# Kernel tuning notes

Hardware: AMD Instinct MI355X
Metric: run time of the kernel (lower is better)

## Reference

```python
import jax, jax.numpy as jnp
import numpy as np

HEADS = 16
HEAD_DIM = 64
LN_EPS = 1e-5


def setup_inputs() -> dict:
    key = jax.random.key(0)
    k_x, k_q, k_k, k_v = jax.random.split(key, 4)
    B, C, H, W = 32, 640, 32, 32
    inner = HEADS * HEAD_DIM  # 1024
    x = jax.random.normal(k_x, (B, C, H, W), dtype=jnp.float32)
    # nn.Linear(in_dim, inner_dim, bias=False): weight shape [inner, in_dim]
    Wq = jax.random.normal(k_q, (inner, C), dtype=jnp.float32) * 0.02
    Wk = jax.random.normal(k_k, (inner, C), dtype=jnp.float32) * 0.02
    Wv = jax.random.normal(k_v, (inner, C), dtype=jnp.float32) * 0.02
    # out_norm = nn.LayerNorm(head_dim): default init gamma=1, beta=0
    gamma = jnp.ones((HEAD_DIM,), dtype=jnp.float32)
    beta = jnp.zeros((HEAD_DIM,), dtype=jnp.float32)
    return {"x": x, "Wq": Wq, "Wk": Wk, "Wv": Wv, "gamma": gamma, "beta": beta}


def _layernorm(y, gamma, beta):
    mu = jnp.mean(y, axis=-1, keepdims=True)
    var = jnp.mean(jnp.square(y - mu), axis=-1, keepdims=True)
    return (y - mu) * jax.lax.rsqrt(var + LN_EPS) * gamma + beta


def reference(x, Wq, Wk, Wv, gamma, beta):
    B, C, H, W = x.shape
    N = H * W
    scale = HEAD_DIM ** -0.5
    # rearrange 'b c h w -> b (h w) c' (patch_size=1)
    t = x.reshape(B, C, N).transpose(0, 2, 1)  # [B, N, C]
    def proj(Wm):
        p = jnp.einsum('bnc,ec->bne', t, Wm)  # [B, N, inner]
        return p.reshape(B, N, HEADS, HEAD_DIM).transpose(0, 2, 1, 3)  # [B, h, N, d]
    q, k, v = proj(Wq), proj(Wk), proj(Wv)
    qk = jnp.einsum('bhid,bhjd->bhij', q, k)  # [B, h, N, N]
    p_att = jax.nn.softmax(qk * scale, axis=-1)
    out = jnp.einsum('bhij,bhjd->bhid', p_att, v)  # [B, h, N, d]
    out = out.mean(axis=2)  # [B, h, d]
    return _layernorm(out, gamma, beta)
```

## Files before the change

### kernel.cpp

```cpp
#include <hip/hip_runtime.h>
#include <hip/hip_bf16.h>

typedef __bf16 bf16;
typedef __bf16 bf16x8 __attribute__((ext_vector_type(8)));
typedef float f32x4 __attribute__((ext_vector_type(4)));

#define QSCALE 0.18033688011112042f

#define EXP2(x) __builtin_amdgcn_exp2f(x)

__device__ __forceinline__ void load_lds16(const void* gp, void* lp) {
  __builtin_amdgcn_global_load_lds((const __attribute__((address_space(1))) void*)gp,
                                   (__attribute__((address_space(3))) void*)lp, 16, 0, 0);
}

__global__ __launch_bounds__(256) void k_transpose(const float* __restrict__ x,
                                                   bf16* __restrict__ t) {
  __shared__ float tile[64][65];
  const int b = blockIdx.z, c0 = blockIdx.y * 64, n0 = blockIdx.x * 64;
  const int tid = threadIdx.x, lx = tid & 63, ly = tid >> 6;
  const float* xp = x + ((size_t)b * 640 + c0) * 1024 + n0;
#pragma unroll
  for (int i = 0; i < 16; ++i) {
    int c = i * 4 + ly;
    tile[c][lx] = xp[(size_t)c * 1024 + lx];
  }
  __syncthreads();
  bf16* tp = t + ((size_t)b * 1024 + n0) * 640 + c0;
#pragma unroll
  for (int i = 0; i < 16; ++i) {
    int n = i * 4 + ly;
    tp[(size_t)n * 640 + lx] = (bf16)tile[lx][n];
  }
}

__global__ __launch_bounds__(256) void k_castw(const float* __restrict__ w,
                                               bf16* __restrict__ dst, float s) {
  int i = blockIdx.x * 256 + threadIdx.x;
  if (i < 655360) dst[i] = (bf16)(w[i] * s);
}

__global__ __launch_bounds__(256) void k_gemm_qkv(const bf16* __restrict__ A,
                                                  const bf16* __restrict__ Bw,
                                                  bf16* __restrict__ qkv) {
  __shared__ __align__(16) bf16 As[128 * 64];
  __shared__ __align__(16) bf16 Bs[128 * 64];
  const int tid = threadIdx.x;
  const int lane = tid & 63;
  const int w = tid >> 6;
  const int wm = w & 1, wn = w >> 1;
  const int g = lane >> 4, ln = lane & 15;
  const int m0 = blockIdx.x * 128;
  const int n0 = blockIdx.y * 128;

  f32x4 acc[4][4];
#pragma unroll
  for (int i = 0; i < 4; ++i)
#pragma unroll
    for (int j = 0; j < 4; ++j)
#pragma unroll
      for (int r = 0; r < 4; ++r) acc[i][j][r] = 0.f;

  for (int k0 = 0; k0 < 640; k0 += 64) {
#pragma unroll
    for (int it = 0; it < 4; ++it) {
      int c = it * 256 + w * 64 + lane;
      int m = c >> 3;
      int kq = (c & 7) ^ (m & 7);
      load_lds16(A + (size_t)(m0 + m) * 640 + (k0 + kq * 8), As + (size_t)(it * 256 + w * 64) * 8);
      load_lds16(Bw + (size_t)(n0 + m) * 640 + (k0 + kq * 8), Bs + (size_t)(it * 256 + w * 64) * 8);
    }
    __syncthreads();
#pragma unroll
    for (int kk = 0; kk < 2; ++kk) {
      bf16x8 af[4], bfr[4];
#pragma unroll
      for (int mi = 0; mi < 4; ++mi) {
        int m = wm * 64 + mi * 16 + ln;
        int cc = m * 8 + ((kk * 4 + g) ^ (m & 7));
        af[mi] = *(const bf16x8*)(As + cc * 8);
      }
#pragma unroll
      for (int ni = 0; ni < 4; ++ni) {
        int n = wn * 64 + ni * 16 + ln;
        int cc = n * 8 + ((kk * 4 + g) ^ (n & 7));
        bfr[ni] = *(const bf16x8*)(Bs + cc * 8);
      }
#pragma unroll
      for (int mi = 0; mi < 4; ++mi)
#pragma unroll
        for (int ni = 0; ni < 4; ++ni)
          acc[mi][ni] = __builtin_amdgcn_mfma_f32_16x16x32_bf16(af[mi], bfr[ni], acc[mi][ni], 0, 0, 0);
    }
    __syncthreads();
  }

#pragma unroll
  for (int mi = 0; mi < 4; ++mi)
#pragma unroll
    for (int ni = 0; ni < 4; ++ni)
#pragma unroll
      for (int r = 0; r < 4; ++r) {
        int row = m0 + wm * 64 + mi * 16 + g * 4 + r;
        int col = n0 + wn * 64 + ni * 16 + ln;
        int bb = row >> 10, n = row & 1023;
        int which = col >> 10, h = (col >> 6) & 15, d = col & 63;
        qkv[(size_t)which * 33554432 +
            ((((size_t)bb * 16 + h) * 1024 + n) * 64 + d)] = (bf16)acc[mi][ni][r];
      }
}

__global__ __launch_bounds__(256) void k_attn(const bf16* __restrict__ q,
                                              const bf16* __restrict__ kmat,
                                              float* __restrict__ wsum) {
  const int bh = blockIdx.y;
  const int it = blockIdx.x;
  const int tid = threadIdx.x;
  const int lane = tid & 63;
  const int w = tid >> 6;
  const int g = lane >> 4, ln = lane & 15;
  const bf16* qb = q + (size_t)bh * 65536;
  const bf16* kb = kmat + (size_t)bh * 65536;
  const int i0 = it * 256 + w * 64;

  bf16x8 qf[4][2];
#pragma unroll
  for (int mi = 0; mi < 4; ++mi)
#pragma unroll
    for (int kc = 0; kc < 2; ++kc)
      qf[mi][kc] = *(const bf16x8*)(qb + (size_t)(i0 + mi * 16 + ln) * 64 + kc * 32 + g * 8);

  float rs[4][4];
#pragma unroll
  for (int mi = 0; mi < 4; ++mi)
#pragma unroll
    for (int r = 0; r < 4; ++r) rs[mi][r] = 0.f;

  for (int jt = 0; jt < 16; ++jt) {
    bf16x8 kf[4][2];
#pragma unroll
    for (int ni = 0; ni < 4; ++ni)
#pragma unroll
      for (int kc = 0; kc < 2; ++kc)
        kf[ni][kc] = *(const bf16x8*)(kb + (size_t)(jt * 64 + ni * 16 + ln) * 64 + kc * 32 + g * 8);
#pragma unroll
    for (int mi = 0; mi < 4; ++mi)
#pragma unroll
      for (int ni = 0; ni < 4; ++ni) {
        f32x4 s = {0.f, 0.f, 0.f, 0.f};
        s = __builtin_amdgcn_mfma_f32_16x16x32_bf16(qf[mi][0], kf[ni][0], s, 0, 0, 0);
        s = __builtin_amdgcn_mfma_f32_16x16x32_bf16(qf[mi][1], kf[ni][1], s, 0, 0, 0);
#pragma unroll
        for (int r = 0; r < 4; ++r) rs[mi][r] += EXP2(s[r]);
      }
  }
  float rinv[4][4];
#pragma unroll
  for (int mi = 0; mi < 4; ++mi)
#pragma unroll
    for (int r = 0; r < 4; ++r) {
      float v = rs[mi][r];
      v += __shfl_xor(v, 1);
      v += __shfl_xor(v, 2);
      v += __shfl_xor(v, 4);
      v += __shfl_xor(v, 8);
      rinv[mi][r] = 1.0f / v;
    }

  for (int jt = 0; jt < 16; ++jt) {
    bf16x8 kf[4][2];
#pragma unroll
    for (int ni = 0; ni < 4; ++ni)
#pragma unroll
      for (int kc = 0; kc < 2; ++kc)
        kf[ni][kc] = *(const bf16x8*)(kb + (size_t)(jt * 64 + ni * 16 + ln) * 64 + kc * 32 + g * 8);
    float cs[4] = {0.f, 0.f, 0.f, 0.f};
#pragma unroll
    for (int mi = 0; mi < 4; ++mi)
#pragma unroll
      for (int ni = 0; ni < 4; ++ni) {
        f32x4 s = {0.f, 0.f, 0.f, 0.f};
        s = __builtin_amdgcn_mfma_f32_16x16x32_bf16(qf[mi][0], kf[ni][0], s, 0, 0, 0);
        s = __builtin_amdgcn_mfma_f32_16x16x32_bf16(qf[mi][1], kf[ni][1], s, 0, 0, 0);
#pragma unroll
        for (int r = 0; r < 4; ++r) cs[ni] += EXP2(s[r]) * rinv[mi][r];
      }
#pragma unroll
    for (int ni = 0; ni < 4; ++ni) {
      float v = cs[ni];
      v += __shfl_xor(v, 16);
      v += __shfl_xor(v, 32);
      if (g == 0) atomicAdd(wsum + (size_t)bh * 1024 + jt * 64 + ni * 16 + ln, v);
    }
  }
}

__global__ __launch_bounds__(256) void k_final(const float* __restrict__ wsum,
                                               const bf16* __restrict__ v,
                                               const float* __restrict__ gamma,
                                               const float* __restrict__ beta,
                                               float* __restrict__ out) {
  const int bh = blockIdx.x;
  const int tid = threadIdx.x;
  const int d = tid & 63, part = tid >> 6;
  const bf16* vb = v + (size_t)bh * 65536;
  const float* wb = wsum + (size_t)bh * 1024;
  float acc = 0.f;
  for (int j = part * 256; j < part * 256 + 256; ++j)
    acc += wb[j] * (float)vb[(size_t)j * 64 + d];
  __shared__ float red[4][64];
  red[part][d] = acc;
  __syncthreads();
  if (tid < 64) {
    float y = (red[0][d] + red[1][d] + red[2][d] + red[3][d]) * (1.0f / 1024.0f);
    float s1 = y;
#pragma unroll
    for (int off = 1; off < 64; off <<= 1) s1 += __shfl_xor(s1, off);
    float mu = s1 * (1.0f / 64.0f);
    float dy = y - mu;
    float s2 = dy * dy;
#pragma unroll
    for (int off = 1; off < 64; off <<= 1) s2 += __shfl_xor(s2, off);
    float rstd = rsqrtf(s2 * (1.0f / 64.0f) + 1e-5f);
    out[(size_t)bh * 64 + d] = dy * rstd * gamma[d] + beta[d];
  }
}

extern "C" void kernel_launch(void* const* d_in, const int* in_sizes, int n_in,
                              void* d_out, int out_size, void* d_ws, size_t ws_size,
                              hipStream_t stream) {
  const float* x     = (const float*)d_in[0];
  const float* Wq    = (const float*)d_in[1];
  const float* Wk    = (const float*)d_in[2];
  const float* Wv    = (const float*)d_in[3];
  const float* gamma = (const float*)d_in[4];
  const float* beta  = (const float*)d_in[5];
  float* out = (float*)d_out;

  char* ws = (char*)d_ws;
  bf16*  tbf  = (bf16*)ws;
  bf16*  wbf  = (bf16*)(ws + 41943040);
  bf16*  qkv  = (bf16*)(ws + 45875200);
  float* wsum = (float*)(ws + 247201792);

  hipMemsetAsync(wsum, 0, (size_t)512 * 1024 * sizeof(float), stream);
  k_transpose<<<dim3(16, 10, 32), 256, 0, stream>>>(x, tbf);
  k_castw<<<2560, 256, 0, stream>>>(Wq, wbf, QSCALE);
  k_castw<<<2560, 256, 0, stream>>>(Wk, wbf + 655360, 1.0f);
  k_castw<<<2560, 256, 0, stream>>>(Wv, wbf + 1310720, 1.0f);
  k_gemm_qkv<<<dim3(256, 24), 256, 0, stream>>>(tbf, wbf, qkv);
  k_attn<<<dim3(4, 512), 256, 0, stream>>>(qkv, qkv + 33554432, wsum);
  k_final<<<512, 256, 0, stream>>>(wsum, qkv + 67108864, gamma, beta, out);
}
```

Baseline: 569.2 us.

## Double-buffer K fragment loads and remap attention blocks for XCD L2 locality

The attention kernel now prefetches the next K tile into a second register buffer while computing on the current one, in both the row-sum pass and the column-weight pass. The grid is flattened and remapped so that the four i-tiles of one batch-head land on the same XCD, which should let them share K reads in that XCD's L2. The double buffer raises register pressure and may lower occupancy.

```diff
diff --git a/kernel.cpp b/kernel.cpp
--- a/kernel.cpp
+++ b/kernel.cpp
@@ -110,11 +110,23 @@
       }
 }
 
+#define LOADK(buf, jt)                                                        \
+  do {                                                                        \
+    const bf16* kp_ = kb + (size_t)(jt) * 4096 + ln * 64 + g * 8;             \
+    _Pragma("unroll") for (int ni_ = 0; ni_ < 4; ++ni_) {                     \
+      buf[ni_ * 2 + 0] = *(const bf16x8*)(kp_ + ni_ * 1024);                  \
+      buf[ni_ * 2 + 1] = *(const bf16x8*)(kp_ + ni_ * 1024 + 32);             \
+    }                                                                         \
+  } while (0)
+
 __global__ __launch_bounds__(256) void k_attn(const bf16* __restrict__ q,
                                               const bf16* __restrict__ kmat,
                                               float* __restrict__ wsum) {
-  const int bh = blockIdx.y;
-  const int it = blockIdx.x;
+  const int idx = blockIdx.x;
+  const int xcd = idx & 7;
+  const int y = idx >> 3;
+  const int it = y & 3;
+  const int bh = xcd + ((y >> 2) << 3);
   const int tid = threadIdx.x;
   const int lane = tid & 63;
   const int w = tid >> 6;
@@ -123,6 +135,8 @@
   const bf16* kb = kmat + (size_t)bh * 65536;
   const int i0 = it * 256 + w * 64;
 
+  const f32x4 zf = {0.f, 0.f, 0.f, 0.f};
+
   bf16x8 qf[4][2];
 #pragma unroll
   for (int mi = 0; mi < 4; ++mi)
@@ -136,20 +150,18 @@
 #pragma unroll
     for (int r = 0; r < 4; ++r) rs[mi][r] = 0.f;
 
+  bf16x8 kbuf[2][8];
+
+  LOADK(kbuf[0], 0);
   for (int jt = 0; jt < 16; ++jt) {
-    bf16x8 kf[4][2];
-#pragma unroll
-    for (int ni = 0; ni < 4; ++ni)
-#pragma unroll
-      for (int kc = 0; kc < 2; ++kc)
-        kf[ni][kc] = *(const bf16x8*)(kb + (size_t)(jt * 64 + ni * 16 + ln) * 64 + kc * 32 + g * 8);
+    if (jt < 15) LOADK(kbuf[(jt + 1) & 1], jt + 1);
+    const bf16x8* kf = kbuf[jt & 1];
 #pragma unroll
     for (int mi = 0; mi < 4; ++mi)
 #pragma unroll
       for (int ni = 0; ni < 4; ++ni) {
-        f32x4 s = {0.f, 0.f, 0.f, 0.f};
-        s = __builtin_amdgcn_mfma_f32_16x16x32_bf16(qf[mi][0], kf[ni][0], s, 0, 0, 0);
-        s = __builtin_amdgcn_mfma_f32_16x16x32_bf16(qf[mi][1], kf[ni][1], s, 0, 0, 0);
+        f32x4 s = __builtin_amdgcn_mfma_f32_16x16x32_bf16(qf[mi][0], kf[ni * 2], zf, 0, 0, 0);
+        s = __builtin_amdgcn_mfma_f32_16x16x32_bf16(qf[mi][1], kf[ni * 2 + 1], s, 0, 0, 0);
 #pragma unroll
         for (int r = 0; r < 4; ++r) rs[mi][r] += EXP2(s[r]);
       }
@@ -167,21 +179,17 @@
       rinv[mi][r] = 1.0f / v;
     }
 
+  LOADK(kbuf[0], 0);
   for (int jt = 0; jt < 16; ++jt) {
-    bf16x8 kf[4][2];
-#pragma unroll
-    for (int ni = 0; ni < 4; ++ni)
-#pragma unroll
-      for (int kc = 0; kc < 2; ++kc)
-        kf[ni][kc] = *(const bf16x8*)(kb + (size_t)(jt * 64 + ni * 16 + ln) * 64 + kc * 32 + g * 8);
+    if (jt < 15) LOADK(kbuf[(jt + 1) & 1], jt + 1);
+    const bf16x8* kf = kbuf[jt & 1];
     float cs[4] = {0.f, 0.f, 0.f, 0.f};
 #pragma unroll
     for (int mi = 0; mi < 4; ++mi)
 #pragma unroll
       for (int ni = 0; ni < 4; ++ni) {
-        f32x4 s = {0.f, 0.f, 0.f, 0.f};
-        s = __builtin_amdgcn_mfma_f32_16x16x32_bf16(qf[mi][0], kf[ni][0], s, 0, 0, 0);
-        s = __builtin_amdgcn_mfma_f32_16x16x32_bf16(qf[mi][1], kf[ni][1], s, 0, 0, 0);
+        f32x4 s = __builtin_amdgcn_mfma_f32_16x16x32_bf16(qf[mi][0], kf[ni * 2], zf, 0, 0, 0);
+        s = __builtin_amdgcn_mfma_f32_16x16x32_bf16(qf[mi][1], kf[ni * 2 + 1], s, 0, 0, 0);
 #pragma unroll
         for (int r = 0; r < 4; ++r) cs[ni] += EXP2(s[r]) * rinv[mi][r];
       }
@@ -249,6 +257,6 @@
   k_castw<<<2560, 256, 0, stream>>>(Wk, wbf + 655360, 1.0f);
   k_castw<<<2560, 256, 0, stream>>>(Wv, wbf + 1310720, 1.0f);
   k_gemm_qkv<<<dim3(256, 24), 256, 0, stream>>>(tbf, wbf, qkv);
-  k_attn<<<dim3(4, 512), 256, 0, stream>>>(qkv, qkv + 33554432, wsum);
+  k_attn<<<2048, 256, 0, stream>>>(qkv, qkv + 33554432, wsum);
   k_final<<<512, 256, 0, stream>>>(wsum, qkv + 67108864, gamma, beta, out);
 }
```

After: 1.014 ms. +78.1%, slower.
